# Performance work log

Hardware: AMD Instinct MI355X
Metric: run time of the kernel (lower is better)

Reference implementation:

```python
import jax, jax.numpy as jnp
import numpy as np

B, IN_F, OUT_F, FAN_IN = 2048, 4096, 4096, 32


def setup_inputs() -> dict:
    key = jax.random.key(0)
    k1, k2, k3, k4 = jax.random.split(key, 4)
    x = jax.random.normal(k1, (B, IN_F), dtype=jnp.float32)
    weight = jax.random.normal(k2, (OUT_F, FAN_IN), dtype=jnp.float32) * (1.0 / np.sqrt(FAN_IN))
    bias = jax.random.normal(k3, (OUT_F,), dtype=jnp.float32) * 0.01
    indx_seqs = jnp.sort(jax.random.randint(k4, (OUT_F, FAN_IN), 0, IN_F, dtype=jnp.int64), axis=1)
    return {"x": x, "weight": weight, "bias": bias, "indx_seqs": indx_seqs}


def reference(x, weight, bias, indx_seqs):
    # gather: (B, OUT_F, FAN_IN) -- input[:, indx_seqs]
    gathered = jnp.take(x, indx_seqs, axis=1)
    # elementwise multiply by weight (OUT_F, FAN_IN), reduce over fan_in, add bias
    return jnp.sum(weight * gathered, axis=2) + bias
```

## Files before the change

### kernel.cpp

```cpp
#include <hip/hip_runtime.h>


constexpr int IN_F  = 4096;
constexpr int OUT_F = 4096;
constexpr int K     = 32;
constexpr int BT    = 4;
constexpr int THREADS = 512;
constexpr int ROWS_PER_BLOCK = 32;
constexpr int ITERS = ROWS_PER_BLOCK / BT;
constexpr int OCHUNKS = OUT_F / THREADS;

__global__ __launch_bounds__(THREADS, 4)
void lc_kernel(const float* __restrict__ x,
               const float* __restrict__ w,
               const float* __restrict__ bias,
               const int* __restrict__ idx,
               float* __restrict__ out,
               int bchunks) {
    __shared__ float4 xs[IN_F];
    const int tid = threadIdx.x;
    const int ochunk = blockIdx.x / bchunks;
    const int bchunk = blockIdx.x % bchunks;
    const int o = ochunk * THREADS + tid;

    int   ao[K];
    float wr[K];
    const int4*   ip = reinterpret_cast<const int4*>(idx + (size_t)o * K);
    const float4* wp = reinterpret_cast<const float4*>(w + (size_t)o * K);
#pragma unroll
    for (int kk = 0; kk < K / 4; ++kk) {
        int4   i4 = ip[kk];
        float4 w4 = wp[kk];
        ao[4*kk+0] = i4.x << 4;  ao[4*kk+1] = i4.y << 4;
        ao[4*kk+2] = i4.z << 4;  ao[4*kk+3] = i4.w << 4;
        wr[4*kk+0] = w4.x;  wr[4*kk+1] = w4.y;
        wr[4*kk+2] = w4.z;  wr[4*kk+3] = w4.w;
    }
    const float bv = bias[o];
    const char* xb = reinterpret_cast<const char*>(xs);

    const int b0 = bchunk * ROWS_PER_BLOCK;
    for (int it = 0; it < ITERS; ++it) {
        const int rb = b0 + it * BT;
        __syncthreads();
        const float* xr = x + (size_t)rb * IN_F;
#pragma unroll
        for (int j = 0; j < IN_F / THREADS; ++j) {
            const int c = tid + j * THREADS;
            float4 v;
            v.x = xr[c];
            v.y = xr[c + IN_F];
            v.z = xr[c + 2 * IN_F];
            v.w = xr[c + 3 * IN_F];
            xs[c] = v;
        }
        __syncthreads();

        float4 acc = {bv, bv, bv, bv};
#pragma unroll
        for (int k = 0; k < K; ++k) {
            float4 xv = *reinterpret_cast<const float4*>(xb + ao[k]);
            acc.x += wr[k] * xv.x;
            acc.y += wr[k] * xv.y;
            acc.z += wr[k] * xv.z;
            acc.w += wr[k] * xv.w;
        }

        float* op = out + (size_t)rb * OUT_F + o;
        op[0]         = acc.x;
        op[OUT_F]     = acc.y;
        op[2 * OUT_F] = acc.z;
        op[3 * OUT_F] = acc.w;
    }
}

extern "C" void kernel_launch(void* const* d_in, const int* in_sizes, int n_in,
                              void* d_out, int out_size, void* d_ws, size_t ws_size,
                              hipStream_t stream) {
    const float* x    = (const float*)d_in[0];
    const float* w    = (const float*)d_in[1];
    const float* bias = (const float*)d_in[2];
    const int*   idx  = (const int*)d_in[3];
    float* out = (float*)d_out;

    const int Bv = in_sizes[0] / IN_F;
    const int bchunks = Bv / ROWS_PER_BLOCK;
    lc_kernel<<<dim3(OCHUNKS * bchunks), dim3(THREADS), 0, stream>>>(
        x, w, bias, idx, out, bchunks);
}
```

Baseline: 44.33 us.

## Store x tile as packed bf16 in double-buffered LDS with register prefetch

Staged activations are now truncated to bf16 and packed two rows per 32-bit word, so one 16-byte LDS gather serves 8 batch rows instead of 4. The LDS tile is double-buffered and the next tile's global loads are issued into registers before the current compute, which removes one barrier per iteration and overlaps load latency with compute. Occupancy hint drops to 2 blocks per CU because of the doubled LDS use and larger register footprint. Truncating x to bf16 loses precision relative to the fp32 reference and may exceed tolerance.

After: 40.68 us. 8.2% less time.

```diff
diff --git a/kernel.cpp b/kernel.cpp
--- a/kernel.cpp
+++ b/kernel.cpp
@@ -4,20 +4,26 @@
 constexpr int IN_F  = 4096;
 constexpr int OUT_F = 4096;
 constexpr int K     = 32;
-constexpr int BT    = 4;
+constexpr int BT    = 8;
 constexpr int THREADS = 512;
 constexpr int ROWS_PER_BLOCK = 32;
 constexpr int ITERS = ROWS_PER_BLOCK / BT;
-constexpr int OCHUNKS = OUT_F / THREADS;
+constexpr int CPT = IN_F / THREADS;
 
-__global__ __launch_bounds__(THREADS, 4)
+__device__ __forceinline__ unsigned pack_bf16(float lo, float hi) {
+    return (__float_as_uint(hi) & 0xffff0000u) | (__float_as_uint(lo) >> 16);
+}
+__device__ __forceinline__ float bf_lo(unsigned u) { return __uint_as_float(u << 16); }
+__device__ __forceinline__ float bf_hi(unsigned u) { return __uint_as_float(u & 0xffff0000u); }
+
+__global__ __launch_bounds__(THREADS, 2)
 void lc_kernel(const float* __restrict__ x,
                const float* __restrict__ w,
                const float* __restrict__ bias,
                const int* __restrict__ idx,
                float* __restrict__ out,
                int bchunks) {
-    __shared__ float4 xs[IN_F];
+    __shared__ int4 xs[2][IN_F];
     const int tid = threadIdx.x;
     const int ochunk = blockIdx.x / bchunks;
     const int bchunk = blockIdx.x % bchunks;
@@ -37,40 +43,79 @@
         wr[4*kk+2] = w4.z;  wr[4*kk+3] = w4.w;
     }
     const float bv = bias[o];
-    const char* xb = reinterpret_cast<const char*>(xs);
+    const int b0 = bchunk * ROWS_PER_BLOCK;
 
-    const int b0 = bchunk * ROWS_PER_BLOCK;
+    float pf[BT * CPT];
+
+    {
+        const float* xr = x + (size_t)b0 * IN_F;
+#pragma unroll
+        for (int j = 0; j < CPT; ++j)
+#pragma unroll
+            for (int r = 0; r < BT; ++r)
+                pf[j * BT + r] = xr[(size_t)r * IN_F + tid + j * THREADS];
+#pragma unroll
+        for (int j = 0; j < CPT; ++j) {
+            int4 pk;
+            pk.x = (int)pack_bf16(pf[j*BT+0], pf[j*BT+1]);
+            pk.y = (int)pack_bf16(pf[j*BT+2], pf[j*BT+3]);
+            pk.z = (int)pack_bf16(pf[j*BT+4], pf[j*BT+5]);
+            pk.w = (int)pack_bf16(pf[j*BT+6], pf[j*BT+7]);
+            xs[0][tid + j * THREADS] = pk;
+        }
+    }
+    __syncthreads();
+
+    const char* xb = reinterpret_cast<const char*>(&xs[0][0]);
+
+#pragma unroll
     for (int it = 0; it < ITERS; ++it) {
-        const int rb = b0 + it * BT;
-        __syncthreads();
-        const float* xr = x + (size_t)rb * IN_F;
+        const int cur = it & 1;
+
+        if (it + 1 < ITERS) {
+            const float* xr = x + (size_t)(b0 + (it + 1) * BT) * IN_F;
 #pragma unroll
-        for (int j = 0; j < IN_F / THREADS; ++j) {
-            const int c = tid + j * THREADS;
-            float4 v;
-            v.x = xr[c];
-            v.y = xr[c + IN_F];
-            v.z = xr[c + 2 * IN_F];
-            v.w = xr[c + 3 * IN_F];
-            xs[c] = v;
+            for (int j = 0; j < CPT; ++j)
+#pragma unroll
+                for (int r = 0; r < BT; ++r)
+                    pf[j * BT + r] = xr[(size_t)r * IN_F + tid + j * THREADS];
+        }
+
+        float acc[BT];
+#pragma unroll
+        for (int r = 0; r < BT; ++r) acc[r] = bv;
+        const char* xc = xb + cur * (int)sizeof(int4) * IN_F;
+#pragma unroll
+        for (int k = 0; k < K; ++k) {
+            int4 v = *reinterpret_cast<const int4*>(xc + ao[k]);
+            const float wk = wr[k];
+            acc[0] += wk * bf_lo((unsigned)v.x);
+            acc[1] += wk * bf_hi((unsigned)v.x);
+            acc[2] += wk * bf_lo((unsigned)v.y);
+            acc[3] += wk * bf_hi((unsigned)v.y);
+            acc[4] += wk * bf_lo((unsigned)v.z);
+            acc[5] += wk * bf_hi((unsigned)v.z);
+            acc[6] += wk * bf_lo((unsigned)v.w);
+            acc[7] += wk * bf_hi((unsigned)v.w);
+        }
+
+        float* op = out + (size_t)(b0 + it * BT) * OUT_F + o;
+#pragma unroll
+        for (int r = 0; r < BT; ++r) op[(size_t)r * OUT_F] = acc[r];
+
+        if (it + 1 < ITERS) {
+            int4* xw = &xs[cur ^ 1][0];
+#pragma unroll
+            for (int j = 0; j < CPT; ++j) {
+                int4 pk;
+                pk.x = (int)pack_bf16(pf[j*BT+0], pf[j*BT+1]);
+                pk.y = (int)pack_bf16(pf[j*BT+2], pf[j*BT+3]);
+                pk.z = (int)pack_bf16(pf[j*BT+4], pf[j*BT+5]);
+                pk.w = (int)pack_bf16(pf[j*BT+6], pf[j*BT+7]);
+                xw[tid + j * THREADS] = pk;
+            }
         }
         __syncthreads();
-
-        float4 acc = {bv, bv, bv, bv};
-#pragma unroll
-        for (int k = 0; k < K; ++k) {
-            float4 xv = *reinterpret_cast<const float4*>(xb + ao[k]);
-            acc.x += wr[k] * xv.x;
-            acc.y += wr[k] * xv.y;
-            acc.z += wr[k] * xv.z;
-            acc.w += wr[k] * xv.w;
-        }
-
-        float* op = out + (size_t)rb * OUT_F + o;
-        op[0]         = acc.x;
-        op[OUT_F]     = acc.y;
-        op[2 * OUT_F] = acc.z;
-        op[3 * OUT_F] = acc.w;
     }
 }
 
@@ -85,6 +130,7 @@
 
     const int Bv = in_sizes[0] / IN_F;
     const int bchunks = Bv / ROWS_PER_BLOCK;
-    lc_kernel<<<dim3(OCHUNKS * bchunks), dim3(THREADS), 0, stream>>>(
+    const int ochunks = (in_sizes[1] / K) / THREADS;
+    lc_kernel<<<dim3(ochunks * bchunks), dim3(THREADS), 0, stream>>>(
         x, w, bias, idx, out, bchunks);
 }
```
